# Kernel tuning notes

Hardware: AMD Instinct MI355X
Metric: run time of the kernel (lower is better)

The kernel has to match this reference:

```python
import jax, jax.numpy as jnp
import numpy as np

B, L, STEPS = 32, 1024, 20


def setup_inputs() -> dict:
    key = jax.random.key(0)
    k0, k1, k2, k3 = jax.random.split(key, 4)
    scores = jax.random.uniform(k0, (B, L, L), dtype=jnp.float32)
    M = jax.random.uniform(k1, (B, L, L), dtype=jnp.float32)  # pairing constraint mask
    rho_p = jax.random.uniform(k2, (L, L), dtype=jnp.float32)
    w = jax.random.uniform(k3, (1,), dtype=jnp.float32)
    return {
        "scores": scores,
        "M": M,
        "rho_p": rho_p,
        "s": jnp.full((1,), 0.5, jnp.float32),
        "w": w,
        "alpha": jnp.full((1,), 0.005, jnp.float32),
        "belt": jnp.full((1,), 0.05, jnp.float32),
        "lr_alpha": jnp.full((1,), 0.99, jnp.float32),
        "lr_belt": jnp.full((1,), 0.99, jnp.float32),
    }


def reference(scores, M, rho_p, s, w, alpha, belt, lr_alpha, lr_belt):
    relu = jax.nn.relu

    def T_A(x):  # symmetrize then mask
        return (x + jnp.swapaxes(x, 1, 2)) * 0.5 * M

    U = scores - s            # (B, L, L)
    A_hat = scores
    A = T_A(A_hat)
    Lm = w * relu(A.sum(-1) - 1.0)  # (B, L) Lagrange multipliers

    def step(carry, t):
        Lm, A, A_hat = carry
        row = A.sum(-1) - 1.0                                  # (B, L)
        G = U * 0.5 - (Lm * jnp.sign(row))[:, :, None]          # broadcast over last dim
        a_t = alpha * lr_alpha ** t                             # (1,) decayed step size
        A_hat = A_hat + a_t * A_hat * M * (G + jnp.swapaxes(G, 1, 2))
        A_hat = relu(jnp.abs(A_hat) - rho_p * a_t)              # soft-threshold
        A_hat = 1.0 - relu(1.0 - A_hat)                         # clip above at 1
        A = T_A(A_hat)
        Lm = Lm + belt * lr_belt ** t * relu(A.sum(-1) - 1.0)   # dual ascent
        return (Lm, A, A_hat), None

    ts = jnp.arange(STEPS, dtype=jnp.float32)
    (Lm, A, A_hat), _ = jax.lax.scan(step, (Lm, A, A_hat), ts)
    return A
```

## Files before the change

### kernel.cpp

```cpp
#include <hip/hip_runtime.h>
#include <hip/hip_fp16.h>
#include <math.h>
#include <type_traits>

#define L 1024
#define BATCH 32
#define TS 64
#define PADF 65
#define PADU 66
#define NT 16
#define NPAIRS 136
#define STEPS 20

struct __align__(8) us4 { unsigned short x, y, z, w; };

__device__ __forceinline__ float4 ld4(const float* p){ return *(const float4*)p; }
__device__ __forceinline__ unsigned short f2bf(float x){
  unsigned int u = __float_as_uint(x);
  u += 0x7fffu + ((u >> 16) & 1u);
  return (unsigned short)(u >> 16);
}
__device__ __forceinline__ float bf2f(unsigned short b){
  return __uint_as_float(((unsigned int)b) << 16);
}
__device__ __forceinline__ unsigned short f2h(float x){
  __half h = __float2half(x);
  return *(unsigned short*)&h;
}
__device__ __forceinline__ float h2f(unsigned short u){
  __half h; *(unsigned short*)&h = u;
  return __half2float(h);
}
template<bool H16> __device__ __forceinline__ float dec16(unsigned short u){
  if constexpr (H16) return h2f(u); else return bf2f(u);
}
__device__ __forceinline__ float red16(float v){
  v += __shfl_xor(v, 1); v += __shfl_xor(v, 2);
  v += __shfl_xor(v, 4); v += __shfl_xor(v, 8);
  return v;
}
__device__ __forceinline__ void decode_pair(int p, int& bi, int& bj){
  bi = 0;
  while (p >= NT - bi){ p -= NT - bi; ++bi; }
  bj = bi + p;
}

__global__ void params_kernel(float* pbuf, const float* s, const float* w,
                              const float* alpha, const float* belt,
                              const float* lra, const float* lrb) {
  int t = threadIdx.x;
  if (t < STEPS) {
    pbuf[t]         = alpha[0] * powf(lra[0], (float)t);
    pbuf[STEPS + t] = belt[0]  * powf(lrb[0], (float)t);
  }
  if (t == 0) { pbuf[2*STEPS] = s[0]; pbuf[2*STEPS + 1] = w[0]; }
}

template<bool PACKM>
__global__ __launch_bounds__(256, 6)
void prep_kernel(const float* __restrict__ scores, const float* __restrict__ Mm,
                 unsigned short* __restrict__ Sb, unsigned short* __restrict__ Mb,
                 float* __restrict__ rsOut, const float* __restrict__ pbuf)
{
  __shared__ float buf1[TS*PADF];
  __shared__ unsigned short buf2[TS*PADU];
  const int b = blockIdx.y;
  int bi, bj; decode_pair(blockIdx.x, bi, bj);
  const bool diag = (bi == bj);
  const int ibase = bi*TS, jbase = bj*TS;
  const int tid = threadIdx.x, cg = tid & 15, rr = tid >> 4, c4 = cg*4;
  const size_t bb = (size_t)b * L * L;
  const float sv = pbuf[2*STEPS];

  #pragma unroll
  for (int it = 0; it < 4; ++it){
    int row = it*16 + rr;
    float4 v = ld4(scores + bb + (size_t)(jbase+row)*L + ibase + c4);
    float* d = &buf1[row*PADF + c4];
    d[0]=v.x; d[1]=v.y; d[2]=v.z; d[3]=v.w;
  }
  __syncthreads();

  #pragma unroll
  for (int it = 0; it < 4; ++it){
    int ii = it*16 + rr;
    size_t off = bb + (size_t)(ibase+ii)*L + jbase + c4;
    float4 s4 = ld4(scores + off);
    float4 m4 = ld4(Mm + off);
    float sc[4] = {s4.x,s4.y,s4.z,s4.w};
    float m [4] = {m4.x,m4.y,m4.z,m4.w};
    unsigned short qs[4], qm[4];
    float part = 0.f;
    #pragma unroll
    for (int k = 0; k < 4; ++k){
      float scT = buf1[(c4+k)*PADF + ii];
      float sbv = 0.5f*(sc[k] + scT) - sv;
      unsigned short q = f2bf(sbv);
      buf2[ii*PADU + c4 + k] = q;
      part += (bf2f(q) + sv) * m[k];
      qs[k] = q; qm[k] = f2bf(m[k]);
    }
    us4 so = {qs[0],qs[1],qs[2],qs[3]};
    *(us4*)(Sb + off) = so;
    if constexpr (PACKM){ us4 mo = {qm[0],qm[1],qm[2],qm[3]}; *(us4*)(Mb + off) = mo; }
    part = red16(part);
    if (cg == 0) rsOut[((size_t)b*NT + bj)*L + ibase + ii] = part;
  }
  __syncthreads();

  if (!diag){
    #pragma unroll
    for (int it = 0; it < 4; ++it){
      int jj = it*16 + rr;
      size_t off = bb + (size_t)(jbase+jj)*L + ibase + c4;
      float4 m4 = ld4(Mm + off);
      float m[4] = {m4.x,m4.y,m4.z,m4.w};
      unsigned short qs[4], qm[4];
      float part = 0.f;
      #pragma unroll
      for (int k = 0; k < 4; ++k){
        unsigned short q = buf2[(c4+k)*PADU + jj];
        part += (bf2f(q) + sv) * m[k];
        qs[k] = q; qm[k] = f2bf(m[k]);
      }
      us4 so = {qs[0],qs[1],qs[2],qs[3]};
      *(us4*)(Sb + off) = so;
      if constexpr (PACKM){ us4 mo = {qm[0],qm[1],qm[2],qm[3]}; *(us4*)(Mb + off) = mo; }
      part = red16(part);
      if (cg == 0) rsOut[((size_t)b*NT + bi)*L + jbase + jj] = part;
    }
  }
}

template<bool PACKM, bool H16, bool FIRST, bool LAST>
__global__ __launch_bounds__(256, LAST ? 4 : 7)
void step_kernel(const float* __restrict__ scores,
                 const unsigned short* __restrict__ Sb,
                 const unsigned short* __restrict__ Mb,
                 const float* __restrict__ Mm,
                 const float* __restrict__ rho,
                 float* __restrict__ Hf,
                 unsigned short* __restrict__ Hh,
                 const float* __restrict__ rsIn, float* __restrict__ rsOut,
                 const float* __restrict__ LmIn, float* __restrict__ LmOut,
                 const float* __restrict__ pbuf, const int t)
{
  using BT = typename std::conditional<LAST, float, unsigned short>::type;
  __shared__ BT bufP[TS*PADU];
  __shared__ BT bufQ[TS*PADU];
  __shared__ float cbuf[2*TS];

  const int b = blockIdx.y;
  int bi, bj; decode_pair(blockIdx.x, bi, bj);
  const bool diag = (bi == bj);
  const int ibase = bi*TS, jbase = bj*TS;
  const int tid = threadIdx.x, cg = tid & 15, rr = tid >> 4, c4 = cg*4;
  const size_t bb = (size_t)b * L * L;
  const float a_t = pbuf[t];

  if (tid < 128){
    const int half = tid >> 6, lane = tid & 63;
    const int rowbase = half ? jbase : ibase;
    const float* rp = rsIn + (size_t)b*NT*L + rowbase + lane;
    float rs = 0.f;
    #pragma unroll
    for (int pq = 0; pq < NT; ++pq) rs += rp[(size_t)pq * L];
    const float rowm = rs - 1.0f;
    const float rl = fmaxf(rowm, 0.f);
    float lm;
    if constexpr (FIRST) lm = pbuf[2*STEPS+1] * rl;
    else lm = LmIn[(size_t)b*L + rowbase + lane] + pbuf[STEPS + t - 1] * rl;
    const float sg = (rowm > 0.f) ? 1.f : ((rowm < 0.f) ? -1.f : 0.f);
    cbuf[tid] = lm * sg;
    if constexpr (!LAST){ if (half == 0) LmOut[(size_t)b*L + rowbase + lane] = lm; }
  }
  __syncthreads();

  float mR[4][4], hnR[4][4], part1[4];

  #pragma unroll
  for (int it = 0; it < 4; ++it){
    const int ii = it*16 + rr;
    const size_t offr = (size_t)(ibase+ii)*L + jbase + c4;
    const size_t off = bb + offr;
    float h[4];
    if constexpr (FIRST){
      float4 h4 = ld4(scores + off); h[0]=h4.x;h[1]=h4.y;h[2]=h4.z;h[3]=h4.w;
    } else if constexpr (H16){
      us4 hu = *(const us4*)(Hh + off);
      h[0]=h2f(hu.x); h[1]=h2f(hu.y); h[2]=h2f(hu.z); h[3]=h2f(hu.w);
    } else {
      float4 h4 = ld4(Hf + off); h[0]=h4.x;h[1]=h4.y;h[2]=h4.z;h[3]=h4.w;
    }
    float m[4];
    if constexpr (LAST){
      float4 m4 = ld4(Mm + off); m[0]=m4.x;m[1]=m4.y;m[2]=m4.z;m[3]=m4.w;
    } else if constexpr (PACKM){
      us4 mu = *(const us4*)(Mb + off);
      m[0]=bf2f(mu.x); m[1]=bf2f(mu.y); m[2]=bf2f(mu.z); m[3]=bf2f(mu.w);
    } else {
      float4 m4 = ld4(Mm + off); m[0]=m4.x;m[1]=m4.y;m[2]=m4.z;m[3]=m4.w;
    }
    us4 su = *(const us4*)(Sb + off);
    float sb[4] = {bf2f(su.x),bf2f(su.y),bf2f(su.z),bf2f(su.w)};
    float4 r4 = ld4(rho + offr);
    float rh[4] = {r4.x,r4.y,r4.z,r4.w};
    const float ci = cbuf[ii];
    float p1 = 0.f;
    unsigned short hb[4];
    float hn[4];
    #pragma unroll
    for (int k = 0; k < 4; ++k){
      const float g = sb[k] - ci - cbuf[TS + c4 + k];
      float x = fmaf(a_t * h[k] * m[k], g, h[k]);
      x = fminf(fmaxf(fabsf(x) - rh[k]*a_t, 0.f), 1.f);
      mR[it][k] = m[k];
      if constexpr (LAST){
        hnR[it][k] = x;
        bufP[ii*PADU + c4 + k] = x;
      } else if constexpr (H16){
        unsigned short bits = f2h(x);
        float xq = h2f(bits);
        hb[k] = bits;
        bufP[ii*PADU + c4 + k] = bits;
        p1 += 0.5f * xq * m[k];
      } else {
        hn[k] = x;
        bufP[ii*PADU + c4 + k] = f2bf(x);
        p1 += 0.5f * x * m[k];
      }
    }
    if constexpr (!LAST){
      part1[it] = p1;
      if constexpr (H16){
        us4 o = {hb[0],hb[1],hb[2],hb[3]};
        *(us4*)(Hh + off) = o;
      } else {
        float4 o; o.x=hn[0]; o.y=hn[1]; o.z=hn[2]; o.w=hn[3];
        *(float4*)(Hf + off) = o;
      }
    }
  }
  __syncthreads();

  if (!diag){
    #pragma unroll
    for (int it = 0; it < 4; ++it){
      const int jj = it*16 + rr;
      const size_t offr = (size_t)(jbase+jj)*L + ibase + c4;
      const size_t off = bb + offr;
      float h[4];
      if constexpr (FIRST){
        float4 h4 = ld4(scores + off); h[0]=h4.x;h[1]=h4.y;h[2]=h4.z;h[3]=h4.w;
      } else if constexpr (H16){
        us4 hu = *(const us4*)(Hh + off);
        h[0]=h2f(hu.x); h[1]=h2f(hu.y); h[2]=h2f(hu.z); h[3]=h2f(hu.w);
      } else {
        float4 h4 = ld4(Hf + off); h[0]=h4.x;h[1]=h4.y;h[2]=h4.z;h[3]=h4.w;
      }
      float m[4];
      if constexpr (LAST){
        float4 m4 = ld4(Mm + off); m[0]=m4.x;m[1]=m4.y;m[2]=m4.z;m[3]=m4.w;
      } else if constexpr (PACKM){
        us4 mu = *(const us4*)(Mb + off);
        m[0]=bf2f(mu.x); m[1]=bf2f(mu.y); m[2]=bf2f(mu.z); m[3]=bf2f(mu.w);
      } else {
        float4 m4 = ld4(Mm + off); m[0]=m4.x;m[1]=m4.y;m[2]=m4.z;m[3]=m4.w;
      }
      us4 su = *(const us4*)(Sb + off);
      float sb[4] = {bf2f(su.x),bf2f(su.y),bf2f(su.z),bf2f(su.w)};
      float4 r4 = ld4(rho + offr);
      float rh[4] = {r4.x,r4.y,r4.z,r4.w};
      const float cj = cbuf[TS + jj];
      float part = 0.f;
      unsigned short hb[4];
      float outv[4];
      #pragma unroll
      for (int k = 0; k < 4; ++k){
        const float g = sb[k] - cj - cbuf[c4 + k];
        float x = fmaf(a_t * h[k] * m[k], g, h[k]);
        x = fminf(fmaxf(fabsf(x) - rh[k]*a_t, 0.f), 1.f);
        if constexpr (LAST){
          float hT = bufP[(c4+k)*PADU + jj];
          outv[k] = 0.5f*(x + hT)*m[k];
          bufQ[jj*PADU + c4 + k] = x;
        } else if constexpr (H16){
          unsigned short bits = f2h(x);
          float xq = h2f(bits);
          hb[k] = bits;
          float hT = h2f(bufP[(c4+k)*PADU + jj]);
          part += 0.5f*(xq + hT)*m[k];
          bufQ[jj*PADU + c4 + k] = bits;
        } else {
          float hT = bf2f(bufP[(c4+k)*PADU + jj]);
          part += 0.5f*(x + hT)*m[k];
          outv[k] = x;
          bufQ[jj*PADU + c4 + k] = f2bf(x);
        }
      }
      if constexpr (LAST){
        float4 o; o.x=outv[0]; o.y=outv[1]; o.z=outv[2]; o.w=outv[3];
        *(float4*)(Hf + off) = o;
      } else if constexpr (H16){
        us4 o = {hb[0],hb[1],hb[2],hb[3]};
        *(us4*)(Hh + off) = o;
      } else {
        float4 o; o.x=outv[0]; o.y=outv[1]; o.z=outv[2]; o.w=outv[3];
        *(float4*)(Hf + off) = o;
      }
      if constexpr (!LAST){
        part = red16(part);
        if (cg == 0) rsOut[((size_t)b*NT + bi)*L + jbase + jj] = part;
      }
    }
  }
  __syncthreads();

  const BT* hs = diag ? bufP : bufQ;
  #pragma unroll
  for (int it = 0; it < 4; ++it){
    const int ii = it*16 + rr;
    if constexpr (LAST){
      float av[4];
      #pragma unroll
      for (int k = 0; k < 4; ++k){
        float hT = hs[(c4+k)*PADU + ii];
        av[k] = 0.5f*(hnR[it][k] + hT)*mR[it][k];
      }
      size_t off = bb + (size_t)(ibase+ii)*L + jbase + c4;
      float4 o; o.x=av[0]; o.y=av[1]; o.z=av[2]; o.w=av[3];
      *(float4*)(Hf + off) = o;
    } else {
      float part = part1[it];
      #pragma unroll
      for (int k = 0; k < 4; ++k)
        part += 0.5f * dec16<H16>(hs[(c4+k)*PADU + ii]) * mR[it][k];
      part = red16(part);
      if (cg == 0) rsOut[((size_t)b*NT + bj)*L + ibase + ii] = part;
    }
  }
}

template<bool PACKM, bool H16>
static void run_steps(const float* scores, const unsigned short* Sb,
                      const unsigned short* Mb, const float* Mm, const float* rho,
                      float* Hf, unsigned short* Hh,
                      float** rs, float** lmv, const float* pbuf, hipStream_t stream)
{
  dim3 grid(NPAIRS, BATCH);
  for (int t = 0; t < STEPS; ++t){
    float* rin = rs[t & 1]; float* rout = rs[(t + 1) & 1];
    const float* lin = lmv[(t + 1) & 1]; float* lout = lmv[t & 1];
    if (t == 0)
      step_kernel<PACKM,H16,true ,false><<<grid,256,0,stream>>>(scores,Sb,Mb,Mm,rho,Hf,Hh,rin,rout,lin,lout,pbuf,t);
    else if (t == STEPS-1)
      step_kernel<PACKM,H16,false,true ><<<grid,256,0,stream>>>(scores,Sb,Mb,Mm,rho,Hf,Hh,rin,rout,lin,lout,pbuf,t);
    else
      step_kernel<PACKM,H16,false,false><<<grid,256,0,stream>>>(scores,Sb,Mb,Mm,rho,Hf,Hh,rin,rout,lin,lout,pbuf,t);
  }
}

extern "C" void kernel_launch(void* const* d_in, const int* in_sizes, int n_in,
                              void* d_out, int out_size, void* d_ws, size_t ws_size,
                              hipStream_t stream) {
  const float* scores = (const float*)d_in[0];
  const float* Mm     = (const float*)d_in[1];
  const float* rho    = (const float*)d_in[2];
  const float* s      = (const float*)d_in[3];
  const float* w      = (const float*)d_in[4];
  const float* alpha  = (const float*)d_in[5];
  const float* belt   = (const float*)d_in[6];
  const float* lra    = (const float*)d_in[7];
  const float* lrb    = (const float*)d_in[8];
  float* Hf = (float*)d_out;

  const size_t SBB = (size_t)BATCH*L*L*2;
  const size_t MBB = (size_t)BATCH*L*L*2;
  const size_t HHB = (size_t)BATCH*L*L*2;
  const size_t RSB = (size_t)BATCH*NT*L*4;
  const size_t LMB = (size_t)BATCH*L*4;
  const size_t need_base = 2*RSB + 2*LMB + 4096;

  char* wp = (char*)d_ws;
  const bool h16   = ws_size >= SBB + MBB + HHB + need_base;
  const bool packm = h16 || (ws_size >= SBB + MBB + need_base);

  size_t off = 0;
  unsigned short* Sb = (unsigned short*)wp; off += SBB;
  unsigned short* Mb = Sb;
  if (packm){ Mb = (unsigned short*)(wp + off); off += MBB; }
  unsigned short* Hh = nullptr;
  if (h16){ Hh = (unsigned short*)(wp + off); off += HHB; }
  float* rs0  = (float*)(wp + off); off += RSB;
  float* rs1  = (float*)(wp + off); off += RSB;
  float* lm0  = (float*)(wp + off); off += LMB;
  float* lm1  = (float*)(wp + off); off += LMB;
  float* pbuf = (float*)(wp + off);

  params_kernel<<<1, 64, 0, stream>>>(pbuf, s, w, alpha, belt, lra, lrb);

  dim3 grid(NPAIRS, BATCH);
  float* rs[2]  = {rs0, rs1};
  float* lmv[2] = {lm0, lm1};

  if (h16){
    prep_kernel<true><<<grid, 256, 0, stream>>>(scores, Mm, Sb, Mb, rs0, pbuf);
    run_steps<true,true>(scores, Sb, Mb, Mm, rho, Hf, Hh, rs, lmv, pbuf, stream);
  } else if (packm){
    prep_kernel<true><<<grid, 256, 0, stream>>>(scores, Mm, Sb, Mb, rs0, pbuf);
    run_steps<true,false>(scores, Sb, Mb, Mm, rho, Hf, Hh, rs, lmv, pbuf, stream);
  } else {
    prep_kernel<false><<<grid, 256, 0, stream>>>(scores, Mm, Sb, Mb, rs0, pbuf);
    run_steps<false,false>(scores, Sb, Mb, Mm, rho, Hf, Hh, rs, lmv, pbuf, stream);
  }
}
```

Measured before the change: 1.259 ms.

## Use persistent grid, fp16 storage, nontemporal output stores and uniform occupancy

Replaces the 2D pair-by-batch grid with a persistent 2048-block grid that loops over tasks, with the batch index taken as the fastest-varying part of the task id. Switches the packed score and mask storage and the shared-memory transpose buffers from bf16 to fp16, including the LAST step, which previously used fp32 shared buffers. Final output writes now use nontemporal stores, and launch bounds are set to 8 waves for all kernels. The aim is to cut shared memory and register pressure, raise occupancy, and lower launch and tail costs. In exchange, fp16 range and precision now apply to scores, the mask and the final transpose values.

```diff
diff --git a/kernel.cpp b/kernel.cpp
--- a/kernel.cpp
+++ b/kernel.cpp
@@ -1,27 +1,24 @@
 #include <hip/hip_runtime.h>
 #include <hip/hip_fp16.h>
 #include <math.h>
-#include <type_traits>
 
 #define L 1024
 #define BATCH 32
 #define TS 64
-#define PADF 65
 #define PADU 66
 #define NT 16
 #define NPAIRS 136
 #define STEPS 20
+#define NTASK (NPAIRS*BATCH)
+#define GRID 2048
 
 struct __align__(8) us4 { unsigned short x, y, z, w; };
+typedef float vf4 __attribute__((ext_vector_type(4)));
 
 __device__ __forceinline__ float4 ld4(const float* p){ return *(const float4*)p; }
-__device__ __forceinline__ unsigned short f2bf(float x){
-  unsigned int u = __float_as_uint(x);
-  u += 0x7fffu + ((u >> 16) & 1u);
-  return (unsigned short)(u >> 16);
-}
-__device__ __forceinline__ float bf2f(unsigned short b){
-  return __uint_as_float(((unsigned int)b) << 16);
+__device__ __forceinline__ void st4_nt(float* p, float a, float b, float c, float d){
+  vf4 v; v.x = a; v.y = b; v.z = c; v.w = d;
+  __builtin_nontemporal_store(v, (vf4*)p);
 }
 __device__ __forceinline__ unsigned short f2h(float x){
   __half h = __float2half(x);
@@ -30,9 +27,6 @@
 __device__ __forceinline__ float h2f(unsigned short u){
   __half h; *(unsigned short*)&h = u;
   return __half2float(h);
-}
-template<bool H16> __device__ __forceinline__ float dec16(unsigned short u){
-  if constexpr (H16) return h2f(u); else return bf2f(u);
 }
 __device__ __forceinline__ float red16(float v){
   v += __shfl_xor(v, 1); v += __shfl_xor(v, 2);
@@ -57,83 +51,87 @@
 }
 
 template<bool PACKM>
-__global__ __launch_bounds__(256, 6)
+__global__ __launch_bounds__(256, 8)
 void prep_kernel(const float* __restrict__ scores, const float* __restrict__ Mm,
                  unsigned short* __restrict__ Sb, unsigned short* __restrict__ Mb,
                  float* __restrict__ rsOut, const float* __restrict__ pbuf)
 {
-  __shared__ float buf1[TS*PADF];
+  __shared__ unsigned short buf1[TS*PADU];
   __shared__ unsigned short buf2[TS*PADU];
-  const int b = blockIdx.y;
-  int bi, bj; decode_pair(blockIdx.x, bi, bj);
-  const bool diag = (bi == bj);
-  const int ibase = bi*TS, jbase = bj*TS;
   const int tid = threadIdx.x, cg = tid & 15, rr = tid >> 4, c4 = cg*4;
-  const size_t bb = (size_t)b * L * L;
   const float sv = pbuf[2*STEPS];
 
-  #pragma unroll
-  for (int it = 0; it < 4; ++it){
-    int row = it*16 + rr;
-    float4 v = ld4(scores + bb + (size_t)(jbase+row)*L + ibase + c4);
-    float* d = &buf1[row*PADF + c4];
-    d[0]=v.x; d[1]=v.y; d[2]=v.z; d[3]=v.w;
-  }
-  __syncthreads();
-
-  #pragma unroll
-  for (int it = 0; it < 4; ++it){
-    int ii = it*16 + rr;
-    size_t off = bb + (size_t)(ibase+ii)*L + jbase + c4;
-    float4 s4 = ld4(scores + off);
-    float4 m4 = ld4(Mm + off);
-    float sc[4] = {s4.x,s4.y,s4.z,s4.w};
-    float m [4] = {m4.x,m4.y,m4.z,m4.w};
-    unsigned short qs[4], qm[4];
-    float part = 0.f;
-    #pragma unroll
-    for (int k = 0; k < 4; ++k){
-      float scT = buf1[(c4+k)*PADF + ii];
-      float sbv = 0.5f*(sc[k] + scT) - sv;
-      unsigned short q = f2bf(sbv);
-      buf2[ii*PADU + c4 + k] = q;
-      part += (bf2f(q) + sv) * m[k];
-      qs[k] = q; qm[k] = f2bf(m[k]);
-    }
-    us4 so = {qs[0],qs[1],qs[2],qs[3]};
-    *(us4*)(Sb + off) = so;
-    if constexpr (PACKM){ us4 mo = {qm[0],qm[1],qm[2],qm[3]}; *(us4*)(Mb + off) = mo; }
-    part = red16(part);
-    if (cg == 0) rsOut[((size_t)b*NT + bj)*L + ibase + ii] = part;
-  }
-  __syncthreads();
-
-  if (!diag){
+  for (int task = blockIdx.x; task < NTASK; task += GRID){
+    const int b = task & (BATCH-1);
+    int bi, bj; decode_pair(task >> 5, bi, bj);
+    const bool diag = (bi == bj);
+    const int ibase = bi*TS, jbase = bj*TS;
+    const size_t bb = (size_t)b * L * L;
+
     #pragma unroll
     for (int it = 0; it < 4; ++it){
-      int jj = it*16 + rr;
-      size_t off = bb + (size_t)(jbase+jj)*L + ibase + c4;
+      int row = it*16 + rr;
+      float4 v = ld4(scores + bb + (size_t)(jbase+row)*L + ibase + c4);
+      unsigned short* d = &buf1[row*PADU + c4];
+      d[0]=f2h(v.x); d[1]=f2h(v.y); d[2]=f2h(v.z); d[3]=f2h(v.w);
+    }
+    __syncthreads();
+
+    #pragma unroll
+    for (int it = 0; it < 4; ++it){
+      int ii = it*16 + rr;
+      size_t off = bb + (size_t)(ibase+ii)*L + jbase + c4;
+      float4 s4 = ld4(scores + off);
       float4 m4 = ld4(Mm + off);
-      float m[4] = {m4.x,m4.y,m4.z,m4.w};
+      float sc[4] = {s4.x,s4.y,s4.z,s4.w};
+      float m [4] = {m4.x,m4.y,m4.z,m4.w};
       unsigned short qs[4], qm[4];
       float part = 0.f;
       #pragma unroll
       for (int k = 0; k < 4; ++k){
-        unsigned short q = buf2[(c4+k)*PADU + jj];
-        part += (bf2f(q) + sv) * m[k];
-        qs[k] = q; qm[k] = f2bf(m[k]);
+        float scT = h2f(buf1[(c4+k)*PADU + ii]);
+        float sbv = 0.5f*(sc[k] + scT) - sv;
+        unsigned short q = f2h(sbv);
+        buf2[ii*PADU + c4 + k] = q;
+        part += (h2f(q) + sv) * m[k];
+        qs[k] = q; qm[k] = f2h(m[k]);
       }
       us4 so = {qs[0],qs[1],qs[2],qs[3]};
       *(us4*)(Sb + off) = so;
       if constexpr (PACKM){ us4 mo = {qm[0],qm[1],qm[2],qm[3]}; *(us4*)(Mb + off) = mo; }
       part = red16(part);
-      if (cg == 0) rsOut[((size_t)b*NT + bi)*L + jbase + jj] = part;
-    }
+      if (cg == 0) rsOut[((size_t)b*NT + bj)*L + ibase + ii] = part;
+    }
+    __syncthreads();
+
+    if (!diag){
+      #pragma unroll
+      for (int it = 0; it < 4; ++it){
+        int jj = it*16 + rr;
+        size_t off = bb + (size_t)(jbase+jj)*L + ibase + c4;
+        float4 m4 = ld4(Mm + off);
+        float m[4] = {m4.x,m4.y,m4.z,m4.w};
+        unsigned short qs[4], qm[4];
+        float part = 0.f;
+        #pragma unroll
+        for (int k = 0; k < 4; ++k){
+          unsigned short q = buf2[(c4+k)*PADU + jj];
+          part += (h2f(q) + sv) * m[k];
+          qs[k] = q; qm[k] = f2h(m[k]);
+        }
+        us4 so = {qs[0],qs[1],qs[2],qs[3]};
+        *(us4*)(Sb + off) = so;
+        if constexpr (PACKM){ us4 mo = {qm[0],qm[1],qm[2],qm[3]}; *(us4*)(Mb + off) = mo; }
+        part = red16(part);
+        if (cg == 0) rsOut[((size_t)b*NT + bi)*L + jbase + jj] = part;
+      }
+    }
+    __syncthreads();
   }
 }
 
 template<bool PACKM, bool H16, bool FIRST, bool LAST>
-__global__ __launch_bounds__(256, LAST ? 4 : 7)
+__global__ __launch_bounds__(256, 8)
 void step_kernel(const float* __restrict__ scores,
                  const unsigned short* __restrict__ Sb,
                  const unsigned short* __restrict__ Mb,
@@ -145,109 +143,44 @@
                  const float* __restrict__ LmIn, float* __restrict__ LmOut,
                  const float* __restrict__ pbuf, const int t)
 {
-  using BT = typename std::conditional<LAST, float, unsigned short>::type;
-  __shared__ BT bufP[TS*PADU];
-  __shared__ BT bufQ[TS*PADU];
+  __shared__ unsigned short bufP[TS*PADU];
+  __shared__ unsigned short bufQ[TS*PADU];
   __shared__ float cbuf[2*TS];
 
-  const int b = blockIdx.y;
-  int bi, bj; decode_pair(blockIdx.x, bi, bj);
-  const bool diag = (bi == bj);
-  const int ibase = bi*TS, jbase = bj*TS;
   const int tid = threadIdx.x, cg = tid & 15, rr = tid >> 4, c4 = cg*4;
-  const size_t bb = (size_t)b * L * L;
   const float a_t = pbuf[t];
 
-  if (tid < 128){
-    const int half = tid >> 6, lane = tid & 63;
-    const int rowbase = half ? jbase : ibase;
-    const float* rp = rsIn + (size_t)b*NT*L + rowbase + lane;
-    float rs = 0.f;
-    #pragma unroll
-    for (int pq = 0; pq < NT; ++pq) rs += rp[(size_t)pq * L];
-    const float rowm = rs - 1.0f;
-    const float rl = fmaxf(rowm, 0.f);
-    float lm;
-    if constexpr (FIRST) lm = pbuf[2*STEPS+1] * rl;
-    else lm = LmIn[(size_t)b*L + rowbase + lane] + pbuf[STEPS + t - 1] * rl;
-    const float sg = (rowm > 0.f) ? 1.f : ((rowm < 0.f) ? -1.f : 0.f);
-    cbuf[tid] = lm * sg;
-    if constexpr (!LAST){ if (half == 0) LmOut[(size_t)b*L + rowbase + lane] = lm; }
-  }
-  __syncthreads();
-
-  float mR[4][4], hnR[4][4], part1[4];
-
-  #pragma unroll
-  for (int it = 0; it < 4; ++it){
-    const int ii = it*16 + rr;
-    const size_t offr = (size_t)(ibase+ii)*L + jbase + c4;
-    const size_t off = bb + offr;
-    float h[4];
-    if constexpr (FIRST){
-      float4 h4 = ld4(scores + off); h[0]=h4.x;h[1]=h4.y;h[2]=h4.z;h[3]=h4.w;
-    } else if constexpr (H16){
-      us4 hu = *(const us4*)(Hh + off);
-      h[0]=h2f(hu.x); h[1]=h2f(hu.y); h[2]=h2f(hu.z); h[3]=h2f(hu.w);
-    } else {
-      float4 h4 = ld4(Hf + off); h[0]=h4.x;h[1]=h4.y;h[2]=h4.z;h[3]=h4.w;
-    }
-    float m[4];
-    if constexpr (LAST){
-      float4 m4 = ld4(Mm + off); m[0]=m4.x;m[1]=m4.y;m[2]=m4.z;m[3]=m4.w;
-    } else if constexpr (PACKM){
-      us4 mu = *(const us4*)(Mb + off);
-      m[0]=bf2f(mu.x); m[1]=bf2f(mu.y); m[2]=bf2f(mu.z); m[3]=bf2f(mu.w);
-    } else {
-      float4 m4 = ld4(Mm + off); m[0]=m4.x;m[1]=m4.y;m[2]=m4.z;m[3]=m4.w;
-    }
-    us4 su = *(const us4*)(Sb + off);
-    float sb[4] = {bf2f(su.x),bf2f(su.y),bf2f(su.z),bf2f(su.w)};
-    float4 r4 = ld4(rho + offr);
-    float rh[4] = {r4.x,r4.y,r4.z,r4.w};
-    const float ci = cbuf[ii];
-    float p1 = 0.f;
-    unsigned short hb[4];
-    float hn[4];
-    #pragma unroll
-    for (int k = 0; k < 4; ++k){
-      const float g = sb[k] - ci - cbuf[TS + c4 + k];
-      float x = fmaf(a_t * h[k] * m[k], g, h[k]);
-      x = fminf(fmaxf(fabsf(x) - rh[k]*a_t, 0.f), 1.f);
-      mR[it][k] = m[k];
-      if constexpr (LAST){
-        hnR[it][k] = x;
-        bufP[ii*PADU + c4 + k] = x;
-      } else if constexpr (H16){
-        unsigned short bits = f2h(x);
-        float xq = h2f(bits);
-        hb[k] = bits;
-        bufP[ii*PADU + c4 + k] = bits;
-        p1 += 0.5f * xq * m[k];
-      } else {
-        hn[k] = x;
-        bufP[ii*PADU + c4 + k] = f2bf(x);
-        p1 += 0.5f * x * m[k];
-      }
-    }
-    if constexpr (!LAST){
-      part1[it] = p1;
-      if constexpr (H16){
-        us4 o = {hb[0],hb[1],hb[2],hb[3]};
-        *(us4*)(Hh + off) = o;
-      } else {
-        float4 o; o.x=hn[0]; o.y=hn[1]; o.z=hn[2]; o.w=hn[3];
-        *(float4*)(Hf + off) = o;
-      }
-    }
-  }
-  __syncthreads();
-
-  if (!diag){
+  for (int task = blockIdx.x; task < NTASK; task += GRID){
+    const int b = task & (BATCH-1);
+    int bi, bj; decode_pair(task >> 5, bi, bj);
+    const bool diag = (bi == bj);
+    const int ibase = bi*TS, jbase = bj*TS;
+    const size_t bb = (size_t)b * L * L;
+
+    if (tid < 128){
+      const int half = tid >> 6, lane = tid & 63;
+      const int rowbase = half ? jbase : ibase;
+      const float* rp = rsIn + (size_t)b*NT*L + rowbase + lane;
+      float rs = 0.f;
+      #pragma unroll
+      for (int pq = 0; pq < NT; ++pq) rs += rp[(size_t)pq * L];
+      const float rowm = rs - 1.0f;
+      const float rl = fmaxf(rowm, 0.f);
+      float lm;
+      if constexpr (FIRST) lm = pbuf[2*STEPS+1] * rl;
+      else lm = LmIn[(size_t)b*L + rowbase + lane] + pbuf[STEPS + t - 1] * rl;
+      const float sg = (rowm > 0.f) ? 1.f : ((rowm < 0.f) ? -1.f : 0.f);
+      cbuf[tid] = lm * sg;
+      if constexpr (!LAST){ if (half == 0) LmOut[(size_t)b*L + rowbase + lane] = lm; }
+    }
+    __syncthreads();
+
+    float mR[4][4], hnR[4][4], part1[4];
+
     #pragma unroll
     for (int it = 0; it < 4; ++it){
-      const int jj = it*16 + rr;
-      const size_t offr = (size_t)(jbase+jj)*L + ibase + c4;
+      const int ii = it*16 + rr;
+      const size_t offr = (size_t)(ibase+ii)*L + jbase + c4;
       const size_t off = bb + offr;
       float h[4];
       if constexpr (FIRST){
@@ -263,81 +196,143 @@
         float4 m4 = ld4(Mm + off); m[0]=m4.x;m[1]=m4.y;m[2]=m4.z;m[3]=m4.w;
       } else if constexpr (PACKM){
         us4 mu = *(const us4*)(Mb + off);
-        m[0]=bf2f(mu.x); m[1]=bf2f(mu.y); m[2]=bf2f(mu.z); m[3]=bf2f(mu.w);
+        m[0]=h2f(mu.x); m[1]=h2f(mu.y); m[2]=h2f(mu.z); m[3]=h2f(mu.w);
       } else {
         float4 m4 = ld4(Mm + off); m[0]=m4.x;m[1]=m4.y;m[2]=m4.z;m[3]=m4.w;
       }
       us4 su = *(const us4*)(Sb + off);
-      float sb[4] = {bf2f(su.x),bf2f(su.y),bf2f(su.z),bf2f(su.w)};
+      float sb[4] = {h2f(su.x),h2f(su.y),h2f(su.z),h2f(su.w)};
       float4 r4 = ld4(rho + offr);
       float rh[4] = {r4.x,r4.y,r4.z,r4.w};
-      const float cj = cbuf[TS + jj];
-      float part = 0.f;
+      const float ci = cbuf[ii];
+      float p1 = 0.f;
       unsigned short hb[4];
-      float outv[4];
+      float hn[4];
       #pragma unroll
       for (int k = 0; k < 4; ++k){
-        const float g = sb[k] - cj - cbuf[c4 + k];
+        const float g = sb[k] - ci - cbuf[TS + c4 + k];
         float x = fmaf(a_t * h[k] * m[k], g, h[k]);
         x = fminf(fmaxf(fabsf(x) - rh[k]*a_t, 0.f), 1.f);
+        mR[it][k] = m[k];
+        unsigned short bits = f2h(x);
+        bufP[ii*PADU + c4 + k] = bits;
         if constexpr (LAST){
-          float hT = bufP[(c4+k)*PADU + jj];
-          outv[k] = 0.5f*(x + hT)*m[k];
-          bufQ[jj*PADU + c4 + k] = x;
+          hnR[it][k] = x;
         } else if constexpr (H16){
-          unsigned short bits = f2h(x);
           float xq = h2f(bits);
           hb[k] = bits;
-          float hT = h2f(bufP[(c4+k)*PADU + jj]);
-          part += 0.5f*(xq + hT)*m[k];
+          p1 += 0.5f * xq * m[k];
+        } else {
+          hn[k] = x;
+          p1 += 0.5f * x * m[k];
+        }
+      }
+      if constexpr (!LAST){
+        part1[it] = p1;
+        if constexpr (H16){
+          us4 o = {hb[0],hb[1],hb[2],hb[3]};
+          *(us4*)(Hh + off) = o;
+        } else {
+          float4 o; o.x=hn[0]; o.y=hn[1]; o.z=hn[2]; o.w=hn[3];
+          *(float4*)(Hf + off) = o;
+        }
+      }
+    }
+    __syncthreads();
+
+    if (!diag){
+      #pragma unroll
+      for (int it = 0; it < 4; ++it){
+        const int jj = it*16 + rr;
+        const size_t offr = (size_t)(jbase+jj)*L + ibase + c4;
+        const size_t off = bb + offr;
+        float h[4];
+        if constexpr (FIRST){
+          float4 h4 = ld4(scores + off); h[0]=h4.x;h[1]=h4.y;h[2]=h4.z;h[3]=h4.w;
+        } else if constexpr (H16){
+          us4 hu = *(const us4*)(Hh + off);
+          h[0]=h2f(hu.x); h[1]=h2f(hu.y); h[2]=h2f(hu.z); h[3]=h2f(hu.w);
+        } else {
+          float4 h4 = ld4(Hf + off); h[0]=h4.x;h[1]=h4.y;h[2]=h4.z;h[3]=h4.w;
+        }
+        float m[4];
+        if constexpr (LAST){
+          float4 m4 = ld4(Mm + off); m[0]=m4.x;m[1]=m4.y;m[2]=m4.z;m[3]=m4.w;
+        } else if constexpr (PACKM){
+          us4 mu = *(const us4*)(Mb + off);
+          m[0]=h2f(mu.x); m[1]=h2f(mu.y); m[2]=h2f(mu.z); m[3]=h2f(mu.w);
+        } else {
+          float4 m4 = ld4(Mm + off); m[0]=m4.x;m[1]=m4.y;m[2]=m4.z;m[3]=m4.w;
+        }
+        us4 su = *(const us4*)(Sb + off);
+        float sb[4] = {h2f(su.x),h2f(su.y),h2f(su.z),h2f(su.w)};
+        float4 r4 = ld4(rho + offr);
+        float rh[4] = {r4.x,r4.y,r4.z,r4.w};
+        const float cj = cbuf[TS + jj];
+        float part = 0.f;
+        unsigned short hb[4];
+        float outv[4];
+        #pragma unroll
+        for (int k = 0; k < 4; ++k){
+          const float g = sb[k] - cj - cbuf[c4 + k];
+          float x = fmaf(a_t * h[k] * m[k], g, h[k]);
+          x = fminf(fmaxf(fabsf(x) - rh[k]*a_t, 0.f), 1.f);
+          unsigned short bits = f2h(x);
           bufQ[jj*PADU + c4 + k] = bits;
+          if constexpr (LAST){
+            float hT = h2f(bufP[(c4+k)*PADU + jj]);
+            outv[k] = 0.5f*(x + hT)*m[k];
+          } else if constexpr (H16){
+            float xq = h2f(bits);
+            hb[k] = bits;
+            float hT = h2f(bufP[(c4+k)*PADU + jj]);
+            part += 0.5f*(xq + hT)*m[k];
+          } else {
+            float hT = h2f(bufP[(c4+k)*PADU + jj]);
+            part += 0.5f*(x + hT)*m[k];
+            outv[k] = x;
+          }
+        }
+        if constexpr (LAST){
+          st4_nt(Hf + off, outv[0], outv[1], outv[2], outv[3]);
+        } else if constexpr (H16){
+          us4 o = {hb[0],hb[1],hb[2],hb[3]};
+          *(us4*)(Hh + off) = o;
         } else {
-          float hT = bf2f(bufP[(c4+k)*PADU + jj]);
-          part += 0.5f*(x + hT)*m[k];
-          outv[k] = x;
-          bufQ[jj*PADU + c4 + k] = f2bf(x);
-        }
-      }
+          float4 o; o.x=outv[0]; o.y=outv[1]; o.z=outv[2]; o.w=outv[3];
+          *(float4*)(Hf + off) = o;
+        }
+        if constexpr (!LAST){
+          part = red16(part);
+          if (cg == 0) rsOut[((size_t)b*NT + bi)*L + jbase + jj] = part;
+        }
+      }
+    }
+    __syncthreads();
+
+    const unsigned short* hs = diag ? bufP : bufQ;
+    #pragma unroll
+    for (int it = 0; it < 4; ++it){
+      const int ii = it*16 + rr;
       if constexpr (LAST){
-        float4 o; o.x=outv[0]; o.y=outv[1]; o.z=outv[2]; o.w=outv[3];
-        *(float4*)(Hf + off) = o;
-      } else if constexpr (H16){
-        us4 o = {hb[0],hb[1],hb[2],hb[3]};
-        *(us4*)(Hh + off) = o;
+        float av[4];
+        #pragma unroll
+        for (int k = 0; k < 4; ++k){
+          float hT = h2f(hs[(c4+k)*PADU + ii]);
+          av[k] = 0.5f*(hnR[it][k] + hT)*mR[it][k];
+        }
+        size_t off = bb + (size_t)(ibase+ii)*L + jbase + c4;
+        st4_nt(Hf + off, av[0], av[1], av[2], av[3]);
       } else {
-        float4 o; o.x=outv[0]; o.y=outv[1]; o.z=outv[2]; o.w=outv[3];
-        *(float4*)(Hf + off) = o;
-      }
-      if constexpr (!LAST){
+        float part = part1[it];
+        #pragma unroll
+        for (int k = 0; k < 4; ++k)
+          part += 0.5f * h2f(hs[(c4+k)*PADU + ii]) * mR[it][k];
         part = red16(part);
-        if (cg == 0) rsOut[((size_t)b*NT + bi)*L + jbase + jj] = part;
-      }
-    }
-  }
-  __syncthreads();
-
-  const BT* hs = diag ? bufP : bufQ;
-  #pragma unroll
-  for (int it = 0; it < 4; ++it){
-    const int ii = it*16 + rr;
-    if constexpr (LAST){
-      float av[4];
-      #pragma unroll
-      for (int k = 0; k < 4; ++k){
-        float hT = hs[(c4+k)*PADU + ii];
-        av[k] = 0.5f*(hnR[it][k] + hT)*mR[it][k];
-      }
-      size_t off = bb + (size_t)(ibase+ii)*L + jbase + c4;
-      float4 o; o.x=av[0]; o.y=av[1]; o.z=av[2]; o.w=av[3];
-      *(float4*)(Hf + off) = o;
-    } else {
-      float part = part1[it];
-      #pragma unroll
-      for (int k = 0; k < 4; ++k)
-        part += 0.5f * dec16<H16>(hs[(c4+k)*PADU + ii]) * mR[it][k];
-      part = red16(part);
-      if (cg == 0) rsOut[((size_t)b*NT + bj)*L + ibase + ii] = part;
-    }
+        if (cg == 0) rsOut[((size_t)b*NT + bj)*L + ibase + ii] = part;
+      }
+    }
+    __syncthreads();
   }
 }
 
@@ -347,16 +342,15 @@
                       float* Hf, unsigned short* Hh,
                       float** rs, float** lmv, const float* pbuf, hipStream_t stream)
 {
-  dim3 grid(NPAIRS, BATCH);
   for (int t = 0; t < STEPS; ++t){
     float* rin = rs[t & 1]; float* rout = rs[(t + 1) & 1];
     const float* lin = lmv[(t + 1) & 1]; float* lout = lmv[t & 1];
     if (t == 0)
-      step_kernel<PACKM,H16,true ,false><<<grid,256,0,stream>>>(scores,Sb,Mb,Mm,rho,Hf,Hh,rin,rout,lin,lout,pbuf,t);
+      step_kernel<PACKM,H16,true ,false><<<GRID,256,0,stream>>>(scores,Sb,Mb,Mm,rho,Hf,Hh,rin,rout,lin,lout,pbuf,t);
     else if (t == STEPS-1)
-      step_kernel<PACKM,H16,false,true ><<<grid,256,0,stream>>>(scores,Sb,Mb,Mm,rho,Hf,Hh,rin,rout,lin,lout,pbuf,t);
+      step_kernel<PACKM,H16,false,true ><<<GRID,256,0,stream>>>(scores,Sb,Mb,Mm,rho,Hf,Hh,rin,rout,lin,lout,pbuf,t);
     else
-      step_kernel<PACKM,H16,false,false><<<grid,256,0,stream>>>(scores,Sb,Mb,Mm,rho,Hf,Hh,rin,rout,lin,lout,pbuf,t);
+      step_kernel<PACKM,H16,false,false><<<GRID,256,0,stream>>>(scores,Sb,Mb,Mm,rho,Hf,Hh,rin,rout,lin,lout,pbuf,t);
   }
 }
 
@@ -399,18 +393,17 @@
 
   params_kernel<<<1, 64, 0, stream>>>(pbuf, s, w, alpha, belt, lra, lrb);
 
-  dim3 grid(NPAIRS, BATCH);
   float* rs[2]  = {rs0, rs1};
   float* lmv[2] = {lm0, lm1};
 
   if (h16){
-    prep_kernel<true><<<grid, 256, 0, stream>>>(scores, Mm, Sb, Mb, rs0, pbuf);
+    prep_kernel<true><<<GRID, 256, 0, stream>>>(scores, Mm, Sb, Mb, rs0, pbuf);
     run_steps<true,true>(scores, Sb, Mb, Mm, rho, Hf, Hh, rs, lmv, pbuf, stream);
   } else if (packm){
-    prep_kernel<true><<<grid, 256, 0, stream>>>(scores, Mm, Sb, Mb, rs0, pbuf);
+    prep_kernel<true><<<GRID, 256, 0, stream>>>(scores, Mm, Sb, Mb, rs0, pbuf);
     run_steps<true,false>(scores, Sb, Mb, Mm, rho, Hf, Hh, rs, lmv, pbuf, stream);
   } else {
-    prep_kernel<false><<<grid, 256, 0, stream>>>(scores, Mm, Sb, Mb, rs0, pbuf);
+    prep_kernel<false><<<GRID, 256, 0, stream>>>(scores, Mm, Sb, Mb, rs0, pbuf);
     run_steps<false,false>(scores, Sb, Mb, Mm, rho, Hf, Hh, rs, lmv, pbuf, stream);
   }
 }
```

Result: slower. 1.641 ms (+30.4%).
